# Performance work log

Measured on AMD Instinct MI355X. Metric: run time of the kernel, lower is better.

Reference implementation:

```python
import math
import jax, jax.numpy as jnp
import numpy as np
from jax import lax

LEAKY_SLOPE = 0.2
ACT_GAIN = math.sqrt(2.0)

def bilinear_filter():
    h = jnp.array([1.0, 3.0, 3.0, 1.0], dtype=jnp.float32)
    h = h[:, None] * h[None, :]
    return h / jnp.sum(h)

def setup_inputs() -> dict:
    key = jax.random.key(0)
    ks = jax.random.split(key, 6)
    B, Cin, Cout, W_DIM, R = 16, 512, 512, 512, 64
    return {
        "x": jax.random.normal(ks[0], (B, Cin, R // 2, R // 2), dtype=jnp.float32),
        "w": jax.random.normal(ks[1], (B, W_DIM), dtype=jnp.float32),
        "noise_raw": jax.random.normal(ks[2], (B, 1, R, R), dtype=jnp.float32),
        "affine_weight": jax.random.normal(ks[3], (Cin, W_DIM), dtype=jnp.float32),
        "affine_bias": jnp.ones((Cin,), dtype=jnp.float32),
        "weight": jax.random.normal(ks[4], (Cout, Cin, 3, 3), dtype=jnp.float32),
        "bias": 0.1 * jax.random.normal(ks[5], (Cout,), dtype=jnp.float32),
        "noise_strength": jnp.float32(1.0),
    }

def reference(x, w, noise_raw, affine_weight, affine_bias, weight, bias, noise_strength):
    B, Cin = x.shape[0], x.shape[1]
    Cout = weight.shape[0]
    w_dim = affine_weight.shape[1]
    # EqualizedLinear affine: weight_gain = 1/sqrt(in), bias_gain = 1, no activation
    styles = w @ (affine_weight * (1.0 / math.sqrt(w_dim))).T + affine_bias  # [B, Cin]
    # demodulation coefficients from modulated weights
    wmod = weight[None] * styles[:, None, :, None, None]                      # [B,Cout,Cin,3,3]
    dcoefs = lax.rsqrt(jnp.sum(jnp.square(wmod), axis=(2, 3, 4)) + 1e-8)     # [B, Cout]
    # modulate input instead of weights
    xs = x * styles[:, :, None, None]
    # up=True path: conv_transpose2d(x, weight.transpose(0,1), stride=2, padding=0)
    # == dilated conv with spatially flipped kernel, pad k-1=2
    w_flip = weight[:, :, ::-1, ::-1]
    y = lax.conv_general_dilated(
        xs, w_flip, window_strides=(1, 1), padding=[(2, 2), (2, 2)],
        lhs_dilation=(2, 2), dimension_numbers=("NCHW", "OIHW", "NCHW"))    # [B,Cout,2H+1,2H+1]
    # filter2d with 4x4 bilinear kernel, gain=4, padding=1 (depthwise)
    f = bilinear_filter() * 4.0
    kd = jnp.tile(f[None, None], (Cout, 1, 1, 1))                            # [Cout,1,4,4]
    y = lax.conv_general_dilated(
        y, kd, window_strides=(1, 1), padding=[(1, 1), (1, 1)],
        dimension_numbers=("NCHW", "OIHW", "NCHW"), feature_group_count=Cout)  # [B,Cout,2H,2H]
    # addcmul: noise + y * dcoefs
    noise = noise_raw * noise_strength
    y = noise + y * dcoefs[:, :, None, None]
    # bias, act gain sqrt(2), leaky relu 0.2
    y = (y + bias[None, :, None, None]) * ACT_GAIN
    return jnp.where(y >= 0, y, LEAKY_SLOPE * y)
```

## Files before the change

kernel.cpp:

```cpp
#include <hip/hip_runtime.h>
#include <hip/hip_bf16.h>
#include <stdint.h>

typedef float f32x4 __attribute__((ext_vector_type(4)));
typedef __bf16 bf16x8 __attribute__((ext_vector_type(8)));

#define GLDS16(gp, lp) __builtin_amdgcn_global_load_lds( \
    (const __attribute__((address_space(1))) void*)(gp), \
    (__attribute__((address_space(3))) void*)(lp), 16, 0, 0)

static __device__ __forceinline__ unsigned short f2bf(float f) {
    unsigned int u = __float_as_uint(f);
    u = (u + 0x7fffu + ((u >> 16) & 1u)) >> 16;
    return (unsigned short)u;
}
static __device__ __forceinline__ float bf2f(unsigned short v) {
    return __uint_as_float(((unsigned int)v) << 16);
}

#define O_STYLES 0
#define O_DCOEF  32768
#define O_XS     65536
#define O_WP     19005440
#define O_Y1     23724032
#define O_WSQ    23724032
#define WS_NEED  96075776
#define SP 1104

__global__ __launch_bounds__(256) void k_styles(const float* __restrict__ w,
                                                const float* __restrict__ aw,
                                                const float* __restrict__ ab,
                                                float* __restrict__ styles) {
    int g = blockIdx.x * 256 + threadIdx.x;
    int b = g >> 9, ci = g & 511;
    const float4* wr = (const float4*)(w + b * 512);
    const float4* ar = (const float4*)(aw + ci * 512);
    float acc = 0.f;
    for (int k = 0; k < 128; ++k) {
        float4 wv = wr[k], av = ar[k];
        acc += wv.x * av.x + wv.y * av.y + wv.z * av.z + wv.w * av.w;
    }
    styles[g] = acc * 0.04419417382415922f + ab[ci];
}

__global__ __launch_bounds__(256) void k_wprep(const float* __restrict__ weight,
                                               float* __restrict__ wsq,
                                               unsigned short* __restrict__ wp) {
    int g = blockIdx.x * 256 + threadIdx.x;
    const float* wb = weight + (long)g * 9;
    float v[9]; float s = 0.f;
#pragma unroll
    for (int t = 0; t < 9; ++t) { v[t] = wb[t]; s += v[t] * v[t]; }
    wsq[g] = s;
    const int wri[9] = {2, 2, 0, 0, 2, 0, 1, 1, 1};
    const int wci[9] = {2, 0, 2, 0, 1, 1, 2, 0, 1};
#pragma unroll
    for (int t = 0; t < 9; ++t)
        wp[t * 262144 + g] = f2bf(v[wri[t] * 3 + wci[t]]);
}

__global__ __launch_bounds__(256) void k_dcoef(const float* __restrict__ styles,
                                               const float* __restrict__ wsq,
                                               float* __restrict__ dcoefs) {
    int g = blockIdx.x * 256 + threadIdx.x;
    int b = g >> 9, co = g & 511;
    const float4* sr = (const float4*)(styles + b * 512);
    const float4* qr = (const float4*)(wsq + co * 512);
    float acc = 1e-8f;
    for (int k = 0; k < 128; ++k) {
        float4 sv = sr[k], qv = qr[k];
        acc += sv.x * sv.x * qv.x + sv.y * sv.y * qv.y + sv.z * sv.z * qv.z + sv.w * sv.w * qv.w;
    }
    dcoefs[g] = rsqrtf(acc);
}

__global__ __launch_bounds__(256) void k_xprep(const float* __restrict__ x,
                                               const float* __restrict__ styles,
                                               unsigned short* __restrict__ xs) {
    __shared__ float T[128][33];
    int bid = blockIdx.x;
    int cc = bid & 3, i = (bid >> 2) & 31, b = bid >> 7;
    int t = threadIdx.x;
    int ci0 = cc * 128;
    int j_r = t & 31, cl_r = t >> 5;
    const float* xp = x + (((long)(b * 512 + ci0)) * 32 + i) * 32;
#pragma unroll
    for (int it = 0; it < 16; ++it) {
        int cl = cl_r + it * 8;
        T[cl][j_r] = xp[cl * 1024 + j_r];
    }
    __syncthreads();
    int ci_w = t & 127, jg = t >> 7;
    float sv = styles[b * 512 + ci0 + ci_w];
    unsigned short* op = xs + (((long)(b * 34 + (i + 1))) * 34 + 1) * 512 + ci0 + ci_w;
#pragma unroll
    for (int jj = 0; jj < 16; ++jj) {
        int j = jg * 16 + jj;
        op[(long)j * 512] = f2bf(T[ci_w][j] * sv);
    }
}

#define ST_A(kk) { GLDS16(xsB + sA0 + akt + (kk)*64, smp + nb + (kk)*16384 + t16); \
                   GLDS16(xsB + sA1 + akt + (kk)*64, smp + nb + (kk)*16384 + t16 + 8192); }
#define ST_B(kk) { GLDS16(wpB + sB0 + bkt + (kk)*64, smp + nb + 32768 + (kk)*16384 + t16); \
                   GLDS16(wpB + sB1 + bkt + (kk)*64, smp + nb + 32768 + (kk)*16384 + t16 + 8192); }
#define PHASE2(kk, STG, TAILBAR) { \
  _Pragma("unroll") for (int i = 0; i < 8; ++i) \
    av[i] = *(const bf16x8*)(smp + cb + (kk)*16384 + abase + (i*16)*64); \
  _Pragma("unroll") for (int j = 0; j < 4; ++j) \
    bv[j] = *(const bf16x8*)(smp + cb + (kk)*16384 + bbase + (j*16)*64); \
  STG; \
  __builtin_amdgcn_sched_barrier(0); \
  asm volatile("s_waitcnt vmcnt(4)" ::: "memory"); \
  __builtin_amdgcn_s_barrier(); \
  asm volatile("s_waitcnt lgkmcnt(0)" ::: "memory"); \
  __builtin_amdgcn_sched_barrier(0); \
  __builtin_amdgcn_s_setprio(1); \
  _Pragma("unroll") for (int i = 0; i < 8; ++i) \
    _Pragma("unroll") for (int j = 0; j < 4; ++j) \
      acc[i][j] = __builtin_amdgcn_mfma_f32_16x16x32_bf16(av[i], bv[j], acc[i][j], 0, 0, 0); \
  __builtin_amdgcn_s_setprio(0); \
  if (TAILBAR) __builtin_amdgcn_s_barrier(); }

__global__ __launch_bounds__(512, 2) void k_conv(const unsigned short* __restrict__ xs,
                                                 const unsigned short* __restrict__ wp,
                                                 unsigned short* __restrict__ y1) {
    extern __shared__ __align__(16) char smem[];
    const unsigned char* xsB = (const unsigned char*)xs;
    const unsigned char* wpB = (const unsigned char*)wp;
    char* smp = smem;

    int d = blockIdx.x;
    int pr, nt;
    if (d >= 544) { int r = d - 544; pr = 272 + (r & 3); nt = r >> 2; }
    else          { pr = (d >> 4) * 8 + (d & 7); nt = (d >> 3) & 1; }
    int par = pr / 69;
    int Mtile = pr - par * 69;
    int Ntile = nt;
    int a_par = par >> 1, c_par = par & 1;
    int ntaps = a_par ? (c_par ? 1 : 2) : (c_par ? 2 : 4);
    int tapofs = (par == 0) ? 0 : ((par == 1) ? 4 : ((par == 2) ? 6 : 8));
    int NKT = ntaps << 3;

    int tid = threadIdx.x;
    int lane = tid & 63, wave = tid >> 6;
    int wm = wave >> 2, wn = wave & 3;
    int lrow = lane & 15;
    int rchunk = (((lane >> 4) ^ ((lrow >> 1) & 3)) << 4);
    int abase = (wm * 128 + lrow) * 64 + rchunk;
    int bbase = 32768 + (wn * 64 + lrow) * 64 + rchunk;

    int srow = tid >> 2;
    int schunk = (((tid & 3) ^ ((tid >> 3) & 3)) << 4);
    int sA0, sA1;
    {
        unsigned gm = (unsigned)(Mtile * 256 + srow);
        if (gm > 17471u) gm = 17471u;
        unsigned b_ = gm / 1092u; unsigned pix = gm - b_ * 1092u;
        unsigned r = pix / 33u; unsigned s = pix - r * 33u;
        sA0 = (int)(((b_ * 34u + r) * 34u + s) << 10) + schunk;
        gm = (unsigned)(Mtile * 256 + srow + 128);
        if (gm > 17471u) gm = 17471u;
        b_ = gm / 1092u; pix = gm - b_ * 1092u;
        r = pix / 33u; s = pix - r * 33u;
        sA1 = (int)(((b_ * 34u + r) * 34u + s) << 10) + schunk;
    }
    int sB0 = ((Ntile * 256 + srow) << 10) + schunk;
    int sB1 = sB0 + (128 << 10);
    int t16 = tid << 4;

    f32x4 acc[8][4];
#pragma unroll
    for (int i = 0; i < 8; ++i)
#pragma unroll
        for (int j = 0; j < 4; ++j)
            acc[i][j] = (f32x4){0.f, 0.f, 0.f, 0.f};
    bf16x8 av[8], bv[4];

    auto mkA = [&](int kt) -> int {
        int tl = kt >> 3; if (tl >= ntaps) tl = ntaps - 1;
        int cib = kt & 7;
        int dio = a_par ? 1 : (c_par ? tl : (tl >> 1));
        int djo = c_par ? 1 : (a_par ? tl : (tl & 1));
        return dio * 34816 + djo * 1024 + cib * 128;
    };
    auto mkB = [&](int kt) -> long {
        int tl = kt >> 3; if (tl >= ntaps) tl = ntaps - 1;
        return (long)(tapofs + tl) * 524288 + (long)((kt & 7) * 128);
    };

    {
        int akt = mkA(0); long bkt = mkB(0); int nb = 0;
        ST_A(0); ST_B(0); ST_A(1); ST_B(1);
    }
    __builtin_amdgcn_sched_barrier(0);
    asm volatile("s_waitcnt vmcnt(4)" ::: "memory");
    __builtin_amdgcn_s_barrier();

    int cur = 0;
    for (int kt = 0; kt < NKT; ++kt) {
        int akt = mkA(kt + 1);
        long bkt = mkB(kt + 1);
        int nb = (cur ^ 1) << 16;
        int cb = cur << 16;
        PHASE2(0, { ST_A(0); ST_B(0); }, 0)
        PHASE2(1, { ST_A(1); ST_B(1); }, 1)
        cur ^= 1;
    }

#pragma unroll
    for (int mf = 0; mf < 8; ++mf) {
        int gm0 = Mtile * 256 + wm * 128 + mf * 16 + ((lane >> 4) << 2);
        if (gm0 < 17472) {
            unsigned ug = (unsigned)gm0;
            unsigned bb = ug / 1092u;
            int pix0 = (int)(ug - bb * 1092u);
            long rowb = ((long)((bb * 4u + par) * 512)) * SP;
#pragma unroll
            for (int nf = 0; nf < 4; ++nf) {
                int co = Ntile * 256 + wn * 64 + nf * 16 + lrow;
                unsigned short* dst = y1 + rowb + (long)co * SP + pix0;
                if (pix0 <= 1084) {
                    ushort4 pk;
                    pk.x = f2bf(acc[mf][nf][0]);
                    pk.y = f2bf(acc[mf][nf][1]);
                    pk.z = f2bf(acc[mf][nf][2]);
                    pk.w = f2bf(acc[mf][nf][3]);
                    *(ushort4*)dst = pk;
                } else if (pix0 == 1088) {
                    dst[0] = f2bf(acc[mf][nf][0]);
                }
            }
        }
    }
}

__global__ __launch_bounds__(256) void k_blur(const unsigned short* __restrict__ y1,
                                              const float* __restrict__ dcoefs,
                                              const float* __restrict__ bias,
                                              const float* __restrict__ noise,
                                              const float* __restrict__ nstr,
                                              float* __restrict__ out) {
    __shared__ float yl[4 * 35 * 36];
    int bid = blockIdx.x;
    int cg = bid & 127, b = bid >> 7;
    int t = threadIdx.x;
    int n = t & 63, mq = t >> 6;
    float ns = nstr[0];

    for (int i = t; i < 5040; i += 256) yl[i] = 0.f;
    __syncthreads();

    const int rvv[4] = {33, 33, 32, 32};
    const float* npb = noise + b * 4096;

    int o = n & 1;
    int se = n >> 1;
    int sp_ = se - 1 + o;
    float a0 = o ? 1.f : 3.f;
    float a1 = o ? 3.f : 1.f;

    for (int cc = 0; cc < 4; ++cc) {
        int co = cg * 4 + cc;
#pragma unroll
        for (int pl = 0; pl < 4; ++pl) {
            const unsigned short* src = y1 + ((long)((b * 4 + pl) * 512 + co)) * SP;
            float* dst = yl + pl * 1260;
            int pv = rvv[pl] * 33;
            for (int it = t; it < 273; it += 256) {
                int p0 = it * 4;
                ushort4 v = *(const ushort4*)(src + p0);
                unsigned short vv[4] = {v.x, v.y, v.z, v.w};
#pragma unroll
                for (int k = 0; k < 4; ++k) {
                    int p = p0 + k;
                    if (p < pv && p < 1089) {
                        unsigned r = (unsigned)p / 33u;
                        unsigned s = (unsigned)p - r * 33u;
                        dst[(r + 1) * 36 + (s + 1)] = bf2f(vv[k]);
                    }
                }
            }
        }
        __syncthreads();

        float dc = dcoefs[b * 512 + co];
        float bi = bias[co];
        float* ob = out + ((long)(b * 512 + co)) * 4096;

        auto H = [&](int ap, int r) -> float {
            const float* pe = yl + (ap * 2) * 1260 + (r + 1) * 36;
            const float* po = pe + 1260;
            return a0 * pe[se + 1] + a1 * pe[se + 2] + a1 * po[sp_ + 1] + a0 * po[sp_ + 2];
        };

        int m0 = mq * 16;
        int re = m0 >> 1;
        float he0 = H(0, re), he1 = H(0, re + 1);
        float ho0 = H(1, re - 1), ho1 = H(1, re);
#pragma unroll
        for (int k = 0; k < 16; k += 2) {
            int m = m0 + k;
            float ve = 3.f * he0 + he1 + ho0 + 3.f * ho1;
            float val = npb[m * 64 + n] * ns + ve * (0.0625f * dc);
            val = (val + bi) * 1.41421356237309515f;
            ob[m * 64 + n] = (val >= 0.f) ? val : 0.2f * val;
            float hn_o = H(1, re + 1);
            float vo = he0 + 3.f * he1 + 3.f * ho1 + hn_o;
            val = npb[(m + 1) * 64 + n] * ns + vo * (0.0625f * dc);
            val = (val + bi) * 1.41421356237309515f;
            ob[(m + 1) * 64 + n] = (val >= 0.f) ? val : 0.2f * val;
            ho0 = ho1; ho1 = hn_o;
            float hn_e = H(0, re + 2);
            he0 = he1; he1 = hn_e;
            re += 1;
        }
        __syncthreads();
    }
}

extern "C" void kernel_launch(void* const* d_in, const int* in_sizes, int n_in,
                              void* d_out, int out_size, void* d_ws, size_t ws_size,
                              hipStream_t stream) {
    (void)in_sizes; (void)n_in; (void)out_size;
    if (ws_size < (size_t)WS_NEED) return;
    const float* x      = (const float*)d_in[0];
    const float* w      = (const float*)d_in[1];
    const float* noise  = (const float*)d_in[2];
    const float* aw     = (const float*)d_in[3];
    const float* ab     = (const float*)d_in[4];
    const float* weight = (const float*)d_in[5];
    const float* bias   = (const float*)d_in[6];
    const float* nstr   = (const float*)d_in[7];
    float* out = (float*)d_out;
    char* ws = (char*)d_ws;
    float* styles          = (float*)(ws + O_STYLES);
    float* dcoefs          = (float*)(ws + O_DCOEF);
    unsigned short* xs     = (unsigned short*)(ws + O_XS);
    unsigned short* wp     = (unsigned short*)(ws + O_WP);
    unsigned short* y1     = (unsigned short*)(ws + O_Y1);
    float* wsq             = (float*)(ws + O_WSQ);

    hipFuncSetAttribute((const void*)k_conv,
                        hipFuncAttributeMaxDynamicSharedMemorySize, 131072);

    hipMemsetAsync(xs, 0, 18939904, stream);
    k_styles<<<32,   256, 0, stream>>>(w, aw, ab, styles);
    k_wprep <<<1024, 256, 0, stream>>>(weight, wsq, wp);
    k_dcoef <<<32,   256, 0, stream>>>(styles, wsq, dcoefs);
    k_xprep <<<2048, 256, 0, stream>>>(x, styles, xs);
    k_conv  <<<552,  512, 131072, stream>>>(xs, wp, y1);
    k_blur  <<<2048, 256, 0, stream>>>(y1, dcoefs, bias, noise, nstr, out);
}
```

Measured before the change: 207.4 us.

## Restructure conv main loop to issue full next-tile prefetch before compute

```diff
diff --git a/kernel.cpp b/kernel.cpp
--- a/kernel.cpp
+++ b/kernel.cpp
@@ -104,23 +104,6 @@
                    GLDS16(xsB + sA1 + akt + (kk)*64, smp + nb + (kk)*16384 + t16 + 8192); }
 #define ST_B(kk) { GLDS16(wpB + sB0 + bkt + (kk)*64, smp + nb + 32768 + (kk)*16384 + t16); \
                    GLDS16(wpB + sB1 + bkt + (kk)*64, smp + nb + 32768 + (kk)*16384 + t16 + 8192); }
-#define PHASE2(kk, STG, TAILBAR) { \
-  _Pragma("unroll") for (int i = 0; i < 8; ++i) \
-    av[i] = *(const bf16x8*)(smp + cb + (kk)*16384 + abase + (i*16)*64); \
-  _Pragma("unroll") for (int j = 0; j < 4; ++j) \
-    bv[j] = *(const bf16x8*)(smp + cb + (kk)*16384 + bbase + (j*16)*64); \
-  STG; \
-  __builtin_amdgcn_sched_barrier(0); \
-  asm volatile("s_waitcnt vmcnt(4)" ::: "memory"); \
-  __builtin_amdgcn_s_barrier(); \
-  asm volatile("s_waitcnt lgkmcnt(0)" ::: "memory"); \
-  __builtin_amdgcn_sched_barrier(0); \
-  __builtin_amdgcn_s_setprio(1); \
-  _Pragma("unroll") for (int i = 0; i < 8; ++i) \
-    _Pragma("unroll") for (int j = 0; j < 4; ++j) \
-      acc[i][j] = __builtin_amdgcn_mfma_f32_16x16x32_bf16(av[i], bv[j], acc[i][j], 0, 0, 0); \
-  __builtin_amdgcn_s_setprio(0); \
-  if (TAILBAR) __builtin_amdgcn_s_barrier(); }
 
 __global__ __launch_bounds__(512, 2) void k_conv(const unsigned short* __restrict__ xs,
                                                  const unsigned short* __restrict__ wp,
@@ -193,19 +176,35 @@
         int akt = mkA(0); long bkt = mkB(0); int nb = 0;
         ST_A(0); ST_B(0); ST_A(1); ST_B(1);
     }
-    __builtin_amdgcn_sched_barrier(0);
-    asm volatile("s_waitcnt vmcnt(4)" ::: "memory");
-    __builtin_amdgcn_s_barrier();
-
-    int cur = 0;
+
     for (int kt = 0; kt < NKT; ++kt) {
         int akt = mkA(kt + 1);
         long bkt = mkB(kt + 1);
-        int nb = (cur ^ 1) << 16;
-        int cb = cur << 16;
-        PHASE2(0, { ST_A(0); ST_B(0); }, 0)
-        PHASE2(1, { ST_A(1); ST_B(1); }, 1)
-        cur ^= 1;
+        int nb = ((kt + 1) & 1) << 16;
+        int cb = (kt & 1) << 16;
+        ST_A(0); ST_B(0); ST_A(1); ST_B(1);
+        __builtin_amdgcn_sched_barrier(0);
+        asm volatile("s_waitcnt vmcnt(8)" ::: "memory");
+        __builtin_amdgcn_s_barrier();
+#pragma unroll
+        for (int kk = 0; kk < 2; ++kk) {
+#pragma unroll
+            for (int i = 0; i < 8; ++i)
+                av[i] = *(const bf16x8*)(smp + cb + kk * 16384 + abase + (i * 16) * 64);
+#pragma unroll
+            for (int j = 0; j < 4; ++j)
+                bv[j] = *(const bf16x8*)(smp + cb + kk * 16384 + bbase + (j * 16) * 64);
+            asm volatile("s_waitcnt lgkmcnt(0)" ::: "memory");
+            __builtin_amdgcn_sched_barrier(0);
+            __builtin_amdgcn_s_setprio(1);
+#pragma unroll
+            for (int i = 0; i < 8; ++i)
+#pragma unroll
+                for (int j = 0; j < 4; ++j)
+                    acc[i][j] = __builtin_amdgcn_mfma_f32_16x16x32_bf16(av[i], bv[j], acc[i][j], 0, 0, 0);
+            __builtin_amdgcn_s_setprio(0);
+        }
+        __builtin_amdgcn_s_barrier();
     }
 
 #pragma unroll
```

Result: slower. 228.0 us (+9.9%).
